# Optimization experiments

Measured on AMD Instinct MI355X. Metric: run time of the kernel, lower is better.

## Reference

```python
import jax, jax.numpy as jnp
import numpy as np

N_NODES = 100000
N_EDGES = 3200000
IN_DIM = 256
UNITS = 128


def setup_inputs() -> dict:
    key = jax.random.key(0)
    k1, k2, k3, k4, k5 = jax.random.split(key, 5)
    x = jax.random.normal(k1, (N_NODES, IN_DIM), dtype=jnp.float32)
    kernel = jax.random.normal(k2, (IN_DIM, UNITS), dtype=jnp.float32) * (1.0 / np.sqrt(IN_DIM))
    adj_rows = jax.random.randint(k3, (N_EDGES,), 0, N_NODES, dtype=jnp.int32)
    adj_cols = jax.random.randint(k4, (N_EDGES,), 0, N_NODES, dtype=jnp.int32)
    adj_vals = jax.random.uniform(k5, (N_EDGES,), dtype=jnp.float32)
    return {"x": x, "kernel": kernel, "adj_rows": adj_rows,
            "adj_cols": adj_cols, "adj_vals": adj_vals}


def reference(x, kernel, adj_rows, adj_cols, adj_vals):
    # Dense transform: [N, in_dim] @ [in_dim, units] -> [N, units]
    h = jnp.matmul(x, kernel)
    # SpMM: out[r] = sum_{edges e with row r} val[e] * h[col[e]]
    msgs = h[adj_cols] * adj_vals[:, None]            # [E, units] gather
    agg = jax.ops.segment_sum(msgs, adj_rows, num_segments=N_NODES)  # scatter-add
    # use_bias=False -> no bias add. Activation: relu.
    return jax.nn.relu(agg)
```

## Files before the change

### kernel.cpp

```cpp
#include <hip/hip_runtime.h>
#include <hip/hip_fp16.h>

#define UNITS 128
#define IN_DIM 256

#define BROWS   98
#define NBPAD   1024
#define NCHUNK  64
#define SEDGE   4272

#define GR   128
#define GKC  64
#define APAD 36
#define BPAD 72

typedef short bf16x8 __attribute__((ext_vector_type(8)));
typedef float f32x4  __attribute__((ext_vector_type(4)));
union FragU { uint4 u; bf16x8 f; };

__device__ inline int bucket_of(int r) {
  return (int)(unsigned)(((unsigned long long)(unsigned)r * 342393ull) >> 25);
}

__device__ inline unsigned short bf16_bits(float a) {
  unsigned u = __float_as_uint(a);
  return (unsigned short)((u + 0x7FFF + ((u >> 16) & 1)) >> 16);
}
__device__ inline unsigned pack_bf16x2(float a, float b) {
  return (unsigned)bf16_bits(a) | ((unsigned)bf16_bits(b) << 16);
}

__global__ __launch_bounds__(256) void wt_kernel(
    const float* __restrict__ W, unsigned short* __restrict__ WT) {
  const int i = blockIdx.x * 256 + threadIdx.x;
  const int k = i >> 7;
  const int n = i & 127;
  WT[n * IN_DIM + k] = bf16_bits(W[i]);
}

__device__ __forceinline__ void do_bin(
    char* smem, int c,
    const int* __restrict__ rows, const int* __restrict__ cols,
    const float* __restrict__ vals, int* __restrict__ cstart,
    int2* __restrict__ binned, int n_edges, int nbuckets, int CS) {
  int* hist = (int*)smem;
  int* aux  = (int*)(smem + NBPAD * 4);
  const int tid = threadIdx.x;
  const int e0 = c * CS;
  const int e_end = min(e0 + CS, n_edges);

  for (int i = tid; i < NBPAD; i += 512) hist[i] = 0;
  __syncthreads();

  for (int e = e0 + tid * 4; e < e_end; e += 2048) {
    const int4 r4 = *(const int4*)(rows + e);
    atomicAdd(&hist[bucket_of(r4.x)], 1);
    atomicAdd(&hist[bucket_of(r4.y)], 1);
    atomicAdd(&hist[bucket_of(r4.z)], 1);
    atomicAdd(&hist[bucket_of(r4.w)], 1);
  }
  __syncthreads();

  const int a0 = hist[2 * tid];
  const int a1 = hist[2 * tid + 1];
  const int p  = a0 + a1;
  aux[tid] = p;
  __syncthreads();
  for (int off = 1; off < 512; off <<= 1) {
    int u = 0;
    if (tid >= off) u = aux[tid - off];
    __syncthreads();
    if (tid >= off) aux[tid] += u;
    __syncthreads();
  }
  const int excl = aux[tid] - p;
  if (2 * tid <= nbuckets) {
    hist[2 * tid] = excl;
    cstart[c * NBPAD + 2 * tid] = excl;
  }
  if (2 * tid + 1 <= nbuckets) {
    hist[2 * tid + 1] = excl + a0;
    cstart[c * NBPAD + 2 * tid + 1] = excl + a0;
  }
  __syncthreads();

  for (int e = e0 + tid * 4; e < e_end; e += 2048) {
    const int4   r4 = *(const int4*)(rows + e);
    const int4   c4 = *(const int4*)(cols + e);
    const float4 v4 = *(const float4*)(vals + e);
#pragma unroll
    for (int u = 0; u < 4; ++u) {
      const int r  = (&r4.x)[u];
      const int b  = bucket_of(r);
      const int rl = r - b * BROWS;
      const int pos = atomicAdd(&hist[b], 1);
      binned[(size_t)c * CS + pos] = make_int2(
          (int)(((unsigned)rl << 25) | ((unsigned)(&c4.x)[u] << 8)),
          __float_as_int((&v4.x)[u]));
    }
  }
}

__device__ __forceinline__ void do_gemm(
    char* smem, int bid,
    const float* __restrict__ x, const unsigned short* __restrict__ WT,
    __half* __restrict__ h, int n_nodes) {
  unsigned*       A_lds = (unsigned*)smem;
  unsigned short* B_lds = (unsigned short*)(smem + 18432);

  const int tid  = threadIdx.x;
  const int lane = tid & 63;
  const int wave = tid >> 6;
  const int row0 = bid * GR;
  const int m    = lane & 15;
  const int quad = lane >> 4;

  f32x4 acc[8];
#pragma unroll
  for (int i = 0; i < 8; ++i) acc[i] = (f32x4){0.f, 0.f, 0.f, 0.f};

  for (int k0 = 0; k0 < IN_DIM; k0 += GKC) {
#pragma unroll
    for (int p = 0; p < 4; ++p) {
      const int idx = tid + p * 512;
      const int rr  = idx >> 4;
      const int c4  = idx & 15;
      const int gr  = row0 + rr;
      float4 v = make_float4(0.f, 0.f, 0.f, 0.f);
      if (gr < n_nodes)
        v = *(const float4*)(x + (size_t)gr * IN_DIM + k0 + c4 * 4);
      unsigned* dst = &A_lds[rr * APAD + c4 * 2];
      dst[0] = pack_bf16x2(v.x, v.y);
      dst[1] = pack_bf16x2(v.z, v.w);
    }
#pragma unroll
    for (int p = 0; p < 2; ++p) {
      const int u = tid + p * 512;
      const int n = u >> 3;
      const int cc = u & 7;
      const uint4 v = *(const uint4*)(WT + (size_t)n * IN_DIM + k0 + cc * 8);
      *(uint4*)&B_lds[n * BPAD + cc * 8] = v;
    }
    __syncthreads();

#pragma unroll
    for (int ks = 0; ks < 2; ++ks) {
      FragU a;
      a.u = *(const uint4*)&A_lds[(wave * 16 + m) * APAD + ks * 16 + quad * 4];
#pragma unroll
      for (int nt = 0; nt < 8; ++nt) {
        FragU b;
        b.u = *(const uint4*)&B_lds[(nt * 16 + m) * BPAD + ks * 32 + quad * 8];
        acc[nt] = __builtin_amdgcn_mfma_f32_16x16x32_bf16(a.f, b.f, acc[nt], 0, 0, 0);
      }
    }
    __syncthreads();
  }

  const int orow = row0 + wave * 16 + quad * 4;
#pragma unroll
  for (int nt = 0; nt < 8; ++nt) {
    const int col = nt * 16 + m;
#pragma unroll
    for (int i = 0; i < 4; ++i) {
      const int rr = orow + i;
      if (rr < n_nodes)
        h[(size_t)rr * UNITS + col] = __float2half(acc[nt][i]);
    }
  }
}

__global__ __launch_bounds__(512) void fused_gemm_bin_kernel(
    const float* __restrict__ x, const unsigned short* __restrict__ WT,
    __half* __restrict__ h,
    const int* __restrict__ rows, const int* __restrict__ cols,
    const float* __restrict__ vals, int* __restrict__ cstart,
    int2* __restrict__ binned, int n_nodes, int n_edges, int nbuckets,
    int CS) {
  __shared__ __align__(16) char smem[36864];
  if (blockIdx.x < NCHUNK)
    do_bin(smem, blockIdx.x, rows, cols, vals, cstart, binned,
           n_edges, nbuckets, CS);
  else
    do_gemm(smem, blockIdx.x - NCHUNK, x, WT, h, n_nodes);
}

#define SA_TPB 512

__global__ __launch_bounds__(SA_TPB) void sortagg_kernel(
    const int* __restrict__ cstart, const int2* __restrict__ binned,
    const __half* __restrict__ h, float* __restrict__ out,
    int n_nodes, int nbuckets, int CS) {
  __shared__ int2 sedge[SEDGE];
  __shared__ int  shist[BROWS];
  __shared__ int  sstart[BROWS + 1];
  __shared__ int  scur[BROWS];
  __shared__ int  sc[NCHUNK];
  __shared__ int  scnt[NCHUNK];

  const int tid  = threadIdx.x;
  const int lane = tid & 63;
  const int wv   = tid >> 6;
  const int b    = blockIdx.x;
  const int row0 = b * BROWS;

  if (tid < NCHUNK) {
    const int s  = cstart[tid * NBPAD + b];
    const int e2 = cstart[tid * NBPAD + b + 1];
    sc[tid]   = s;
    scnt[tid] = e2 - s;
  }
  for (int i = tid; i < SEDGE; i += SA_TPB) sedge[i] = make_int2(0, 0);
  if (tid < BROWS) shist[tid] = 0;
  __syncthreads();

#pragma unroll 1
  for (int k = 0; k < 8; ++k) {
    const int c   = wv * 8 + k;
    const int cnt = scnt[c];
    const size_t base = (size_t)c * CS + sc[c];
    for (int j = lane; j < cnt; j += 64)
      atomicAdd(&shist[(unsigned)binned[base + j].x >> 25], 1);
  }
  __syncthreads();

  if (wv == 0) {
    const int v0 = shist[lane];
    const int p0 = (v0 + 7) & ~7;
    int s = p0;
#pragma unroll
    for (int off = 1; off < 64; off <<= 1) {
      const int u = __shfl_up(s, off, 64);
      if (lane >= off) s += u;
    }
    sstart[lane] = s - p0;
    scur[lane]   = s - p0;
    const int t0 = __shfl(s, 63, 64);
    const int idx = 64 + lane;
    const int v1 = (idx < BROWS) ? shist[idx] : 0;
    const int p1 = (idx < BROWS) ? ((v1 + 7) & ~7) : 0;
    int s1 = p1;
#pragma unroll
    for (int off = 1; off < 64; off <<= 1) {
      const int u = __shfl_up(s1, off, 64);
      if (lane >= off) s1 += u;
    }
    if (idx < BROWS) {
      sstart[idx] = t0 + s1 - p1;
      scur[idx]   = t0 + s1 - p1;
    }
    if (lane == 63) sstart[BROWS] = t0 + s1;
  }
  __syncthreads();

#pragma unroll 1
  for (int k = 0; k < 8; ++k) {
    const int c   = wv * 8 + k;
    const int cnt = scnt[c];
    const size_t base = (size_t)c * CS + sc[c];
    for (int j = lane; j < cnt; j += 64) {
      const int2 q = binned[base + j];
      const int rl = (unsigned)q.x >> 25;
      const int pos = atomicAdd(&scur[rl], 1);
      sedge[pos] = make_int2(q.x & 0x01FFFF00, q.y);
    }
  }
  __syncthreads();

  const char* hb = (const char*)h + (lane << 2);
#pragma unroll 1
  for (int i = 0; i < 13; ++i) {
    const int rl = wv + i * 8;
    if (rl >= BROWS) break;
    const int row = row0 + rl;
    if (row >= n_nodes) break;
    const int s = sstart[rl];
    const int e = sstart[rl + 1];
    float accx = 0.f, accy = 0.f;
    for (int j = s; j < e; j += 8) {
      float v[8]; float2 f[8];
#pragma unroll
      for (int u = 0; u < 8; ++u) {
        const int2 q = sedge[j + u];
        v[u] = __int_as_float(q.y);
        f[u] = __half22float2(*(const __half2*)(hb + (unsigned)q.x));
      }
#pragma unroll
      for (int u = 0; u < 8; ++u) {
        accx = fmaf(v[u], f[u].x, accx);
        accy = fmaf(v[u], f[u].y, accy);
      }
    }
    float2 o;
    o.x = accx > 0.f ? accx : 0.f;
    o.y = accy > 0.f ? accy : 0.f;
    ((float2*)(out + (size_t)row * UNITS))[lane] = o;
  }
}

extern "C" void kernel_launch(void* const* d_in, const int* in_sizes, int n_in,
                              void* d_out, int out_size, void* d_ws, size_t ws_size,
                              hipStream_t stream) {
  const float* x     = (const float*)d_in[0];
  const float* W     = (const float*)d_in[1];
  const int*   rows  = (const int*)d_in[2];
  const int*   cols  = (const int*)d_in[3];
  const float* vals  = (const float*)d_in[4];
  float*       out   = (float*)d_out;

  const int n_nodes = in_sizes[0] / IN_DIM;
  const int n_edges = in_sizes[2];
  const int nbuckets = (n_nodes + BROWS - 1) / BROWS;
  const int CS = ((n_edges + NCHUNK - 1) / NCHUNK + 3) & ~3;

  char* ws = (char*)d_ws;
  size_t off = 0;
  auto alloc = [&](size_t bytes) {
    char* p = ws + off;
    off += (bytes + 511) & ~(size_t)511;
    return p;
  };
  __half*         h      = (__half*)alloc((size_t)n_nodes * UNITS * sizeof(__half));
  unsigned short* WT     = (unsigned short*)alloc((size_t)UNITS * IN_DIM * 2);
  int*            cstart = (int*)   alloc((size_t)NCHUNK * NBPAD * sizeof(int));
  int2*           binned = (int2*)  alloc((size_t)NCHUNK * CS * sizeof(int2));

  wt_kernel<<<(IN_DIM * UNITS) / 256, 256, 0, stream>>>(W, WT);

  const int ntiles = (n_nodes + GR - 1) / GR;
  fused_gemm_bin_kernel<<<NCHUNK + ntiles, 512, 0, stream>>>(
      x, WT, h, rows, cols, vals, cstart, binned, n_nodes, n_edges, nbuckets, CS);

  sortagg_kernel<<<nbuckets, SA_TPB, 0, stream>>>(
      cstart, binned, h, out, n_nodes, nbuckets, CS);
}
```

Baseline: 401.0 us.

## Bin edges into fixed-capacity per-bucket slots via global atomic counters

```diff
diff --git a/kernel.cpp b/kernel.cpp
--- a/kernel.cpp
+++ b/kernel.cpp
@@ -5,14 +5,17 @@
 #define IN_DIM 256
 
 #define BROWS   98
-#define NBPAD   1024
-#define NCHUNK  64
-#define SEDGE   4272
+#define NBUCK   1021
+#define BCAP    3584
+#define SEDGE   4288
+#define NCHUNK  256
+#define CS      12500
 
 #define GR   128
 #define GKC  64
 #define APAD 36
 #define BPAD 72
+#define NGEMM 768
 
 typedef short bf16x8 __attribute__((ext_vector_type(8)));
 typedef float f32x4  __attribute__((ext_vector_type(4)));
@@ -31,7 +34,12 @@
 }
 
 __global__ __launch_bounds__(256) void wt_kernel(
-    const float* __restrict__ W, unsigned short* __restrict__ WT) {
+    const float* __restrict__ W, unsigned short* __restrict__ WT,
+    int* __restrict__ bcount) {
+  if (blockIdx.x == 128) {
+    for (int i = threadIdx.x; i < NBUCK; i += 256) bcount[i] = 0;
+    return;
+  }
   const int i = blockIdx.x * 256 + threadIdx.x;
   const int k = i >> 7;
   const int n = i & 127;
@@ -41,49 +49,28 @@
 __device__ __forceinline__ void do_bin(
     char* smem, int c,
     const int* __restrict__ rows, const int* __restrict__ cols,
-    const float* __restrict__ vals, int* __restrict__ cstart,
-    int2* __restrict__ binned, int n_edges, int nbuckets, int CS) {
-  int* hist = (int*)smem;
-  int* aux  = (int*)(smem + NBPAD * 4);
+    const float* __restrict__ vals, int* __restrict__ bcount,
+    int2* __restrict__ binned, int n_edges) {
+  int* sh_cnt = (int*)smem;
   const int tid = threadIdx.x;
   const int e0 = c * CS;
   const int e_end = min(e0 + CS, n_edges);
 
-  for (int i = tid; i < NBPAD; i += 512) hist[i] = 0;
-  __syncthreads();
-
+  for (int i = tid; i < NBUCK; i += 512) sh_cnt[i] = 0;
+  __syncthreads();
   for (int e = e0 + tid * 4; e < e_end; e += 2048) {
     const int4 r4 = *(const int4*)(rows + e);
-    atomicAdd(&hist[bucket_of(r4.x)], 1);
-    atomicAdd(&hist[bucket_of(r4.y)], 1);
-    atomicAdd(&hist[bucket_of(r4.z)], 1);
-    atomicAdd(&hist[bucket_of(r4.w)], 1);
-  }
-  __syncthreads();
-
-  const int a0 = hist[2 * tid];
-  const int a1 = hist[2 * tid + 1];
-  const int p  = a0 + a1;
-  aux[tid] = p;
-  __syncthreads();
-  for (int off = 1; off < 512; off <<= 1) {
-    int u = 0;
-    if (tid >= off) u = aux[tid - off];
-    __syncthreads();
-    if (tid >= off) aux[tid] += u;
-    __syncthreads();
-  }
-  const int excl = aux[tid] - p;
-  if (2 * tid <= nbuckets) {
-    hist[2 * tid] = excl;
-    cstart[c * NBPAD + 2 * tid] = excl;
-  }
-  if (2 * tid + 1 <= nbuckets) {
-    hist[2 * tid + 1] = excl + a0;
-    cstart[c * NBPAD + 2 * tid + 1] = excl + a0;
-  }
-  __syncthreads();
-
+    atomicAdd(&sh_cnt[bucket_of(r4.x)], 1);
+    atomicAdd(&sh_cnt[bucket_of(r4.y)], 1);
+    atomicAdd(&sh_cnt[bucket_of(r4.z)], 1);
+    atomicAdd(&sh_cnt[bucket_of(r4.w)], 1);
+  }
+  __syncthreads();
+  for (int i = tid; i < NBUCK; i += 512) {
+    const int cc = sh_cnt[i];
+    sh_cnt[i] = cc ? atomicAdd(&bcount[i], cc) : 0;
+  }
+  __syncthreads();
   for (int e = e0 + tid * 4; e < e_end; e += 2048) {
     const int4   r4 = *(const int4*)(rows + e);
     const int4   c4 = *(const int4*)(cols + e);
@@ -93,10 +80,11 @@
       const int r  = (&r4.x)[u];
       const int b  = bucket_of(r);
       const int rl = r - b * BROWS;
-      const int pos = atomicAdd(&hist[b], 1);
-      binned[(size_t)c * CS + pos] = make_int2(
-          (int)(((unsigned)rl << 25) | ((unsigned)(&c4.x)[u] << 8)),
-          __float_as_int((&v4.x)[u]));
+      const int pos = atomicAdd(&sh_cnt[b], 1);
+      if (pos < BCAP)
+        binned[(size_t)b * BCAP + pos] = make_int2(
+            (int)(((unsigned)rl << 25) | ((unsigned)(&c4.x)[u] << 8)),
+            __float_as_int((&v4.x)[u]));
     }
   }
 }
@@ -174,29 +162,31 @@
     const float* __restrict__ x, const unsigned short* __restrict__ WT,
     __half* __restrict__ h,
     const int* __restrict__ rows, const int* __restrict__ cols,
-    const float* __restrict__ vals, int* __restrict__ cstart,
-    int2* __restrict__ binned, int n_nodes, int n_edges, int nbuckets,
-    int CS) {
+    const float* __restrict__ vals, int* __restrict__ bcount,
+    int2* __restrict__ binned, int n_nodes, int n_edges) {
   __shared__ __align__(16) char smem[36864];
-  if (blockIdx.x < NCHUNK)
-    do_bin(smem, blockIdx.x, rows, cols, vals, cstart, binned,
-           n_edges, nbuckets, CS);
-  else
-    do_gemm(smem, blockIdx.x - NCHUNK, x, WT, h, n_nodes);
+  const int bid = blockIdx.x;
+  if (bid < NCHUNK) {
+    do_bin(smem, bid, rows, cols, vals, bcount, binned, n_edges);
+  } else {
+    const int t = bid - NCHUNK;
+    do_gemm(smem, t, x, WT, h, n_nodes);
+    if (t < 14) {
+      __syncthreads();
+      do_gemm(smem, NGEMM + t, x, WT, h, n_nodes);
+    }
+  }
 }
 
 #define SA_TPB 512
 
 __global__ __launch_bounds__(SA_TPB) void sortagg_kernel(
-    const int* __restrict__ cstart, const int2* __restrict__ binned,
-    const __half* __restrict__ h, float* __restrict__ out,
-    int n_nodes, int nbuckets, int CS) {
+    const int* __restrict__ bcount, const int2* __restrict__ binned,
+    const __half* __restrict__ h, float* __restrict__ out, int n_nodes) {
   __shared__ int2 sedge[SEDGE];
   __shared__ int  shist[BROWS];
   __shared__ int  sstart[BROWS + 1];
   __shared__ int  scur[BROWS];
-  __shared__ int  sc[NCHUNK];
-  __shared__ int  scnt[NCHUNK];
 
   const int tid  = threadIdx.x;
   const int lane = tid & 63;
@@ -204,23 +194,27 @@
   const int b    = blockIdx.x;
   const int row0 = b * BROWS;
 
-  if (tid < NCHUNK) {
-    const int s  = cstart[tid * NBPAD + b];
-    const int e2 = cstart[tid * NBPAD + b + 1];
-    sc[tid]   = s;
-    scnt[tid] = e2 - s;
-  }
-  for (int i = tid; i < SEDGE; i += SA_TPB) sedge[i] = make_int2(0, 0);
+  int cnt = bcount[b]; if (cnt > BCAP) cnt = BCAP;
+
+  int2 my[7];
+#pragma unroll
+  for (int k = 0; k < 7; ++k) {
+    const int j = tid + k * SA_TPB;
+    my[k] = (j < cnt) ? binned[(size_t)b * BCAP + j] : make_int2(0, 0);
+  }
+
+#pragma unroll
+  for (int k = 0; k < 9; ++k) {
+    const int i = tid + k * SA_TPB;
+    if (i < SEDGE) sedge[i] = make_int2(0, 0);
+  }
   if (tid < BROWS) shist[tid] = 0;
   __syncthreads();
 
-#pragma unroll 1
-  for (int k = 0; k < 8; ++k) {
-    const int c   = wv * 8 + k;
-    const int cnt = scnt[c];
-    const size_t base = (size_t)c * CS + sc[c];
-    for (int j = lane; j < cnt; j += 64)
-      atomicAdd(&shist[(unsigned)binned[base + j].x >> 25], 1);
+#pragma unroll
+  for (int k = 0; k < 7; ++k) {
+    const int j = tid + k * SA_TPB;
+    if (j < cnt) atomicAdd(&shist[(unsigned)my[k].x >> 25], 1);
   }
   __syncthreads();
 
@@ -253,16 +247,13 @@
   }
   __syncthreads();
 
-#pragma unroll 1
-  for (int k = 0; k < 8; ++k) {
-    const int c   = wv * 8 + k;
-    const int cnt = scnt[c];
-    const size_t base = (size_t)c * CS + sc[c];
-    for (int j = lane; j < cnt; j += 64) {
-      const int2 q = binned[base + j];
-      const int rl = (unsigned)q.x >> 25;
+#pragma unroll
+  for (int k = 0; k < 7; ++k) {
+    const int j = tid + k * SA_TPB;
+    if (j < cnt) {
+      const int rl  = (unsigned)my[k].x >> 25;
       const int pos = atomicAdd(&scur[rl], 1);
-      sedge[pos] = make_int2(q.x & 0x01FFFF00, q.y);
+      sedge[pos] = make_int2(my[k].x & 0x01FFFF00, my[k].y);
     }
   }
   __syncthreads();
@@ -310,8 +301,6 @@
 
   const int n_nodes = in_sizes[0] / IN_DIM;
   const int n_edges = in_sizes[2];
-  const int nbuckets = (n_nodes + BROWS - 1) / BROWS;
-  const int CS = ((n_edges + NCHUNK - 1) / NCHUNK + 3) & ~3;
 
   char* ws = (char*)d_ws;
   size_t off = 0;
@@ -322,15 +311,13 @@
   };
   __half*         h      = (__half*)alloc((size_t)n_nodes * UNITS * sizeof(__half));
   unsigned short* WT     = (unsigned short*)alloc((size_t)UNITS * IN_DIM * 2);
-  int*            cstart = (int*)   alloc((size_t)NCHUNK * NBPAD * sizeof(int));
-  int2*           binned = (int2*)  alloc((size_t)NCHUNK * CS * sizeof(int2));
-
-  wt_kernel<<<(IN_DIM * UNITS) / 256, 256, 0, stream>>>(W, WT);
-
-  const int ntiles = (n_nodes + GR - 1) / GR;
-  fused_gemm_bin_kernel<<<NCHUNK + ntiles, 512, 0, stream>>>(
-      x, WT, h, rows, cols, vals, cstart, binned, n_nodes, n_edges, nbuckets, CS);
-
-  sortagg_kernel<<<nbuckets, SA_TPB, 0, stream>>>(
-      cstart, binned, h, out, n_nodes, nbuckets, CS);
-}
+  int*            bcount = (int*)   alloc((size_t)NBUCK * sizeof(int));
+  int2*           binned = (int2*)  alloc((size_t)NBUCK * BCAP * sizeof(int2));
+
+  wt_kernel<<<129, 256, 0, stream>>>(W, WT, bcount);
+
+  fused_gemm_bin_kernel<<<NCHUNK + NGEMM, 512, 0, stream>>>(
+      x, WT, h, rows, cols, vals, bcount, binned, n_nodes, n_edges);
+
+  sortagg_kernel<<<NBUCK, SA_TPB, 0, stream>>>(bcount, binned, h, out, n_nodes);
+}
```

Result: faster. 359.8 us (-10.3%).
